# Performance work log

Hardware: AMD Instinct MI355X
Metric: run time of the kernel (lower is better)

Reference implementation:

```python
import jax, jax.numpy as jnp
import numpy as np

B, S, D_IN, D_OUT = 4, 2048, 4096, 16384


def setup_inputs() -> dict:
    key = jax.random.key(0)
    k1, k2, k3, k4 = jax.random.split(key, 4)
    x = jax.random.normal(k1, (B, S, D_IN), dtype=jnp.float32)
    # per-channel symmetric int8 weights, [out_features, in_features]
    weight_int8 = jax.random.randint(k2, (D_OUT, D_IN), -128, 128, dtype=jnp.int32).astype(jnp.int8)
    # per-channel weight scales (positive, realistic magnitude)
    weight_scale = jax.random.uniform(k3, (D_OUT,), dtype=jnp.float32) * 0.01 + 1e-4
    # static per-tensor activation scale (calibrated constant)
    act_scale = jnp.float32(0.02)
    bias = jax.random.normal(k4, (D_OUT,), dtype=jnp.float32) * 0.1
    return {"x": x, "weight_int8": weight_int8, "weight_scale": weight_scale,
            "act_scale": act_scale, "bias": bias}


def reference(x, weight_int8, weight_scale, act_scale, bias):
    orig_shape = x.shape
    orig_dtype = x.dtype
    x2d = x.reshape(-1, orig_shape[-1])  # [M, D_in]
    # static per-tensor symmetric activation quantization
    x_int8 = jnp.clip(jnp.round(x2d.astype(jnp.float32) / act_scale), -128, 127).astype(jnp.int8)
    y_int32 = jnp.matmul(x_int8, weight_int8.T, preferred_element_type=jnp.int32)  # [M, D_out]
    output_scale = (act_scale * weight_scale).astype(jnp.float32)  # [D_out]
    y = y_int32.astype(jnp.float32) * output_scale[None, :] + bias.astype(jnp.float32)[None, :]
    return y.reshape(*orig_shape[:-1], y.shape[-1]).astype(orig_dtype)
```

## Files before the change

### kernel.cpp

```cpp
#include <hip/hip_runtime.h>
#include <stdint.h>

#define GAS __attribute__((address_space(1)))
#define LAS __attribute__((address_space(3)))

typedef int v4i  __attribute__((ext_vector_type(4)));
typedef int v16i __attribute__((ext_vector_type(16)));

constexpr int Mdim = 8192;
constexpr int Ndim = 16384;
constexpr int Kdim = 4096;

__device__ __forceinline__ int pack4i8(int a, int b, int c, int d) {
    return (a & 255) | ((b & 255) << 8) | ((c & 255) << 16) | ((d & 255) << 24);
}

__device__ __forceinline__ int qz(float v, float inv) {
    return (int)fminf(fmaxf(rintf(v * inv), -128.0f), 127.0f);
}

__global__ void k_quant_x(const float* __restrict__ x, const float* __restrict__ asc,
                          int8_t* __restrict__ xq) {
    const int i = blockIdx.x * blockDim.x + threadIdx.x;
    const float inv = 1.0f / *asc;
    const float4* xv = (const float4*)x + (size_t)i * 4;
    float4 f0 = xv[0], f1 = xv[1], f2 = xv[2], f3 = xv[3];
    int4 o;
    o.x = pack4i8(qz(f0.x, inv), qz(f0.y, inv), qz(f0.z, inv), qz(f0.w, inv));
    o.y = pack4i8(qz(f1.x, inv), qz(f1.y, inv), qz(f1.z, inv), qz(f1.w, inv));
    o.z = pack4i8(qz(f2.x, inv), qz(f2.y, inv), qz(f2.z, inv), qz(f2.w, inv));
    o.w = pack4i8(qz(f3.x, inv), qz(f3.y, inv), qz(f3.z, inv), qz(f3.w, inv));
    ((int4*)xq)[i] = o;
}

__global__ void k_conv_w(const int* __restrict__ w, int8_t* __restrict__ wq) {
    const int i = blockIdx.x * blockDim.x + threadIdx.x;
    const int4* wv = (const int4*)w + (size_t)i * 4;
    int4 a = wv[0], b = wv[1], c = wv[2], d = wv[3];
    int4 o;
    o.x = pack4i8(a.x, a.y, a.z, a.w);
    o.y = pack4i8(b.x, b.y, b.z, b.w);
    o.z = pack4i8(c.x, c.y, c.z, c.w);
    o.w = pack4i8(d.x, d.y, d.z, d.w);
    ((int4*)wq)[i] = o;
}


#define VM0 asm volatile("s_waitcnt vmcnt(0)" ::: "memory")

#define RD(BUF, KS, AA, BB)                                                    \
  {                                                                            \
    _Pragma("unroll") for (int i_ = 0; i_ < 4; ++i_)                           \
      AA[i_] = *(const v4i*)(lds + (BUF) + arow + i_ * 4096 + kso[KS]);        \
    _Pragma("unroll") for (int i_ = 0; i_ < 4; ++i_)                           \
      BB[i_] = *(const v4i*)(lds + 65536 + (BUF) + brow + i_ * 4096 + kso[KS]);\
  }

#define MM(AA, BB)                                                             \
  {                                                                            \
    __builtin_amdgcn_s_setprio(1);                                             \
    _Pragma("unroll") for (int mi_ = 0; mi_ < 4; ++mi_)                        \
      _Pragma("unroll") for (int ni_ = 0; ni_ < 4; ++ni_)                      \
        acc[mi_][ni_] = __builtin_amdgcn_mfma_i32_32x32x32_i8(                 \
            AA[mi_], BB[ni_], acc[mi_][ni_], 0, 0, 0);                         \
    __builtin_amdgcn_s_setprio(0);                                             \
  }

#define TILE(T, B0, DOSTG, DORD)                                               \
  {                                                                            \
    __builtin_amdgcn_s_barrier();                                              \
    __builtin_amdgcn_sched_barrier(0);                                         \
    if (DOSTG) stage((T) + 1);                                                 \
    RD(B0, 1, aQ, bQ)                                                          \
    MM(aP, bP)                                                                 \
    RD(B0, 2, aP, bP)                                                          \
    MM(aQ, bQ)                                                                 \
    RD(B0, 3, aQ, bQ)                                                          \
    MM(aP, bP)                                                                 \
    if (DORD) {                                                                \
      VM0;                                                                     \
      __builtin_amdgcn_s_barrier();                                            \
      __builtin_amdgcn_sched_barrier(0);                                       \
      RD((B0) ^ 32768, 0, aP, bP)                                              \
    }                                                                          \
    MM(aQ, bQ)                                                                 \
  }

__global__ __launch_bounds__(256, 1)
void k_gemm32(const int8_t* __restrict__ Aq, const int8_t* __restrict__ Bq,
              const float* __restrict__ wscale, const float* __restrict__ asc,
              const float* __restrict__ bias, float* __restrict__ out) {
    __shared__ __align__(16) int8_t lds[131072];
    const int tid = threadIdx.x, lane = tid & 63, w = tid >> 6;
    const int wm = w >> 1, wn = w & 1;
    const int l5 = lane & 31, lhi = lane >> 5, llo = lane & 7;

    const int bid = blockIdx.x;
    const int swz = ((bid & 7) << 8) | (bid >> 3);
    const int mt = swz & 31, nt = swz >> 5;
    const int m0 = mt << 8, n0 = nt << 8;

    const int srow = tid >> 3;
    const int scol = (((tid & 7) ^ (srow & 7)) << 4);
    const int8_t* gA = Aq + (size_t)(m0 + srow) * Kdim + scol;
    const int8_t* gB = Bq + (size_t)(n0 + srow) * Kdim + scol;
    const size_t ustep = (size_t)32 * Kdim;
    const int dst0 = w << 10;

    auto stage = [&](int t) {
        const int buf = (t & 1) << 15;
        const int kb = t << 7;
#pragma unroll
        for (int u = 0; u < 8; ++u)
            __builtin_amdgcn_global_load_lds((const GAS void*)(gA + u * ustep + kb),
                                             (LAS void*)(lds + buf + u * 4096 + dst0), 16, 0, 0);
#pragma unroll
        for (int u = 0; u < 8; ++u)
            __builtin_amdgcn_global_load_lds((const GAS void*)(gB + u * ustep + kb),
                                             (LAS void*)(lds + 65536 + buf + u * 4096 + dst0), 16, 0, 0);
    };

    const int arow = (wm * 128 + l5) * 128;
    const int brow = (wn * 128 + l5) * 128;
    int kso[4];
#pragma unroll
    for (int ks = 0; ks < 4; ++ks) kso[ks] = (((ks * 2 + lhi) ^ llo) << 4);

    v16i acc[4][4];
#pragma unroll
    for (int i = 0; i < 4; ++i)
#pragma unroll
        for (int j = 0; j < 4; ++j)
#pragma unroll
            for (int r = 0; r < 16; ++r) acc[i][j][r] = 0;

    v4i aP[4], bP[4], aQ[4], bQ[4];

    stage(0);
    VM0;
    __builtin_amdgcn_s_barrier();
    __builtin_amdgcn_sched_barrier(0);
    RD(0, 0, aP, bP)

    for (int tt = 0; tt < 15; ++tt) {
        const int t2 = tt * 2;
        TILE(t2,     0,     1, 1)
        TILE(t2 + 1, 32768, 1, 1)
    }
    TILE(30, 0,     1, 1)
    TILE(31, 32768, 0, 0)

    const float ascale = *asc;
#pragma unroll
    for (int ni = 0; ni < 4; ++ni) {
        const int col = n0 + wn * 128 + ni * 32 + l5;
        const float sc = ascale * wscale[col];
        const float bb = bias[col];
#pragma unroll
        for (int mi = 0; mi < 4; ++mi) {
            const int rbase = m0 + wm * 128 + mi * 32 + 4 * lhi;
#pragma unroll
            for (int r = 0; r < 16; ++r) {
                const int row = rbase + (r & 3) + 8 * (r >> 2);
                out[(size_t)row * Ndim + col] = (float)acc[mi][ni][r] * sc + bb;
            }
        }
    }
}

template <bool AQ>
__global__ __launch_bounds__(256)
void k_gemm(const int8_t* __restrict__ Aq, const float* __restrict__ Xf,
            const int* __restrict__ W32,
            const float* __restrict__ wscale, const float* __restrict__ asc,
            const float* __restrict__ bias, float* __restrict__ out) {
    constexpr int BM = 128, BN = 128, BK = 64;
    constexpr int KT = Kdim / BK;
    __shared__ __align__(16) int8_t As[2][BM * BK];
    __shared__ __align__(16) int8_t Bs[2][BN * BK];

    const int tid  = threadIdx.x;
    const int lane = tid & 63;
    const int wid  = tid >> 6;
    const int wm = wid >> 1, wn = wid & 1;
    const int lrow = lane & 15, kgrp = lane >> 4;

    const int cpx = gridDim.x >> 3;
    const int swz = ((int)blockIdx.x & 7) * cpx + ((int)blockIdx.x >> 3);
    const int mt = swz & (Mdim / BM - 1);
    const int nt = swz / (Mdim / BM);
    const int m0 = mt * BM, n0 = nt * BN;

    const float ascale = *asc;
    const float inv = 1.0f / ascale;

    v4i acc[4][4];
#pragma unroll
    for (int i = 0; i < 4; ++i)
#pragma unroll
        for (int j = 0; j < 4; ++j) acc[i][j] = (v4i){0, 0, 0, 0};

    auto stg = [&](int buf, int kt) {
        const int k0 = kt * BK;
        if constexpr (AQ) {
            int8_t* ldsp = &As[buf][wid << 10];
            const int8_t* g = Aq + (size_t)(m0 + (tid >> 2)) * Kdim + k0 + ((tid & 3) << 4);
            __builtin_amdgcn_global_load_lds((const GAS void*)g, (LAS void*)ldsp, 16, 0, 0);
            __builtin_amdgcn_global_load_lds((const GAS void*)(g + (size_t)64 * Kdim),
                                             (LAS void*)(ldsp + 4096), 16, 0, 0);
        } else {
            const int row = tid >> 1, cb = (tid & 1) << 5;
            const float4* src = (const float4*)(Xf + (size_t)(m0 + row) * Kdim + k0 + cb);
            int t[8];
#pragma unroll
            for (int j = 0; j < 8; ++j) {
                float4 f = src[j];
                t[j] = pack4i8(qz(f.x, inv), qz(f.y, inv), qz(f.z, inv), qz(f.w, inv));
            }
            int4* dst = (int4*)&As[buf][row * BK + cb];
            dst[0] = make_int4(t[0], t[1], t[2], t[3]);
            dst[1] = make_int4(t[4], t[5], t[6], t[7]);
        }
        {
            const int row = tid >> 1, cb = (tid & 1) << 5;
            const int4* src = (const int4*)(W32 + (size_t)(n0 + row) * Kdim + k0 + cb);
            int t[8];
#pragma unroll
            for (int j = 0; j < 8; ++j) {
                int4 vv = src[j];
                t[j] = pack4i8(vv.x, vv.y, vv.z, vv.w);
            }
            int4* dst = (int4*)&Bs[buf][row * BK + cb];
            dst[0] = make_int4(t[0], t[1], t[2], t[3]);
            dst[1] = make_int4(t[4], t[5], t[6], t[7]);
        }
    };

    stg(0, 0);
    for (int kt = 0; kt < KT; ++kt) {
        const int cur = kt & 1;
        __syncthreads();
        if (kt + 1 < KT) stg(cur ^ 1, kt + 1);

        v4i a[4], b[4];
        const int koff = kgrp << 4;
#pragma unroll
        for (int i = 0; i < 4; ++i) {
            a[i] = *(const v4i*)&As[cur][(wm * 64 + i * 16 + lrow) * BK + koff];
            b[i] = *(const v4i*)&Bs[cur][(wn * 64 + i * 16 + lrow) * BK + koff];
        }
#pragma unroll
        for (int i = 0; i < 4; ++i)
#pragma unroll
            for (int j = 0; j < 4; ++j)
                acc[i][j] = __builtin_amdgcn_mfma_i32_16x16x64_i8(a[i], b[j], acc[i][j], 0, 0, 0);
    }

#pragma unroll
    for (int j = 0; j < 4; ++j) {
        const int col = n0 + wn * 64 + j * 16 + lrow;
        const float sc = ascale * wscale[col];
        const float bb = bias[col];
#pragma unroll
        for (int i = 0; i < 4; ++i) {
            const int r0 = m0 + wm * 64 + i * 16 + (kgrp << 2);
            float* o = out + (size_t)r0 * Ndim + col;
#pragma unroll
            for (int r = 0; r < 4; ++r)
                o[(size_t)r * Ndim] = (float)acc[i][j][r] * sc + bb;
        }
    }
}

extern "C" void kernel_launch(void* const* d_in, const int* in_sizes, int n_in,
                              void* d_out, int out_size, void* d_ws, size_t ws_size,
                              hipStream_t stream) {
    const float* x      = (const float*)d_in[0];
    const int*   w32    = (const int*)d_in[1];
    const float* wscale = (const float*)d_in[2];
    const float* asc    = (const float*)d_in[3];
    const float* bias   = (const float*)d_in[4];
    float* out = (float*)d_out;

    const size_t nx = (size_t)Mdim * Kdim;
    const size_t nw = (size_t)Ndim * Kdim;
    int8_t* xq = (int8_t*)d_ws;
    int8_t* wq = xq + nx;

    const bool haveX = ws_size >= nx;
    const bool haveW = ws_size >= nx + nw;

    if (haveX) k_quant_x<<<(int)(nx / 16 / 256), 256, 0, stream>>>(x, asc, xq);
    if (haveW) k_conv_w<<<(int)(nw / 16 / 256), 256, 0, stream>>>(w32, wq);

    if (haveW) {
        dim3 grid((Mdim / 256) * (Ndim / 256));
        k_gemm32<<<grid, 256, 0, stream>>>(xq, wq, wscale, asc, bias, out);
    } else if (haveX) {
        dim3 grid((Mdim / 128) * (Ndim / 128));
        k_gemm<true><<<grid, 256, 0, stream>>>(xq, x, w32, wscale, asc, bias, out);
    } else {
        dim3 grid((Mdim / 128) * (Ndim / 128));
        k_gemm<false><<<grid, 256, 0, stream>>>(xq, x, w32, wscale, asc, bias, out);
    }
}
```

Before: 770.6 us.

## Pre-pack operands into MFMA fragment order and stream from global to registers

The quantize and weight-convert kernels now write int8 data already laid out as per-lane MFMA fragments, in 1 KB chunks per 32-row, 32-k group. The GEMM drops its LDS staging, barriers and swizzled LDS reads. Each wave instead loads its fragments straight from global memory into registers, using a 4-deep software-pipelined register ring. This removes LDS traffic and synchronisation, but each wave loads its own copy of A and B, so operands are no longer shared between waves through LDS and global/L2 traffic rises. Latency hiding now relies only on the register prefetch distance.

```diff
diff --git a/kernel.cpp b/kernel.cpp
--- a/kernel.cpp
+++ b/kernel.cpp
@@ -10,6 +10,7 @@
 constexpr int Mdim = 8192;
 constexpr int Ndim = 16384;
 constexpr int Kdim = 4096;
+constexpr int KS   = Kdim / 32;
 
 __device__ __forceinline__ int pack4i8(int a, int b, int c, int d) {
     return (a & 255) | ((b & 255) << 8) | ((c & 255) << 16) | ((d & 255) << 24);
@@ -17,6 +18,40 @@
 
 __device__ __forceinline__ int qz(float v, float inv) {
     return (int)fminf(fmaxf(rintf(v * inv), -128.0f), 127.0f);
+}
+
+__global__ void k_quant_xf(const float* __restrict__ x, const float* __restrict__ asc,
+                           int8_t* __restrict__ xq) {
+    const int e = blockIdx.x * blockDim.x + threadIdx.x;
+    const float inv = 1.0f / *asc;
+    const int lane = e & 63, cidx = e >> 6;
+    const int ks = cidx & (KS - 1), mt32 = cidx >> 7;
+    const int row = (mt32 << 5) + (lane & 31);
+    const int k   = (ks << 5) + ((lane >> 5) << 4);
+    const float4* src = (const float4*)(x + (size_t)row * Kdim + k);
+    float4 f0 = src[0], f1 = src[1], f2 = src[2], f3 = src[3];
+    int4 o;
+    o.x = pack4i8(qz(f0.x, inv), qz(f0.y, inv), qz(f0.z, inv), qz(f0.w, inv));
+    o.y = pack4i8(qz(f1.x, inv), qz(f1.y, inv), qz(f1.z, inv), qz(f1.w, inv));
+    o.z = pack4i8(qz(f2.x, inv), qz(f2.y, inv), qz(f2.z, inv), qz(f2.w, inv));
+    o.w = pack4i8(qz(f3.x, inv), qz(f3.y, inv), qz(f3.z, inv), qz(f3.w, inv));
+    ((int4*)xq)[e] = o;
+}
+
+__global__ void k_pack_wf(const int* __restrict__ w, int8_t* __restrict__ wp) {
+    const int e = blockIdx.x * blockDim.x + threadIdx.x;
+    const int lane = e & 63, cidx = e >> 6;
+    const int ks = cidx & (KS - 1), nt32 = cidx >> 7;
+    const int n = (nt32 << 5) + (lane & 31);
+    const int k = (ks << 5) + ((lane >> 5) << 4);
+    const int4* src = (const int4*)(w + (size_t)n * Kdim + k);
+    int4 a = src[0], b = src[1], c = src[2], d = src[3];
+    int4 o;
+    o.x = pack4i8(a.x, a.y, a.z, a.w);
+    o.y = pack4i8(b.x, b.y, b.z, b.w);
+    o.z = pack4i8(c.x, c.y, c.z, c.w);
+    o.w = pack4i8(d.x, d.y, d.z, d.w);
+    ((int4*)wp)[e] = o;
 }
 
 __global__ void k_quant_x(const float* __restrict__ x, const float* __restrict__ asc,
@@ -33,98 +68,40 @@
     ((int4*)xq)[i] = o;
 }
 
-__global__ void k_conv_w(const int* __restrict__ w, int8_t* __restrict__ wq) {
-    const int i = blockIdx.x * blockDim.x + threadIdx.x;
-    const int4* wv = (const int4*)w + (size_t)i * 4;
-    int4 a = wv[0], b = wv[1], c = wv[2], d = wv[3];
-    int4 o;
-    o.x = pack4i8(a.x, a.y, a.z, a.w);
-    o.y = pack4i8(b.x, b.y, b.z, b.w);
-    o.z = pack4i8(c.x, c.y, c.z, c.w);
-    o.w = pack4i8(d.x, d.y, d.z, d.w);
-    ((int4*)wq)[i] = o;
-}
-
-
-#define VM0 asm volatile("s_waitcnt vmcnt(0)" ::: "memory")
-
-#define RD(BUF, KS, AA, BB)                                                    \
+
+#define LOADP(SET, G)                                                          \
   {                                                                            \
-    _Pragma("unroll") for (int i_ = 0; i_ < 4; ++i_)                           \
-      AA[i_] = *(const v4i*)(lds + (BUF) + arow + i_ * 4096 + kso[KS]);        \
-    _Pragma("unroll") for (int i_ = 0; i_ < 4; ++i_)                           \
-      BB[i_] = *(const v4i*)(lds + 65536 + (BUF) + brow + i_ * 4096 + kso[KS]);\
+    _Pragma("unroll") for (int q_ = 0; q_ < 4; ++q_)                           \
+      SET##a[q_] = *(const v4i*)(Apk + (((size_t)(arow32 + q_ * KS8) + (G)) << 10) + lob); \
+    _Pragma("unroll") for (int q_ = 0; q_ < 4; ++q_)                           \
+      SET##b[q_] = *(const v4i*)(Bpk + (((size_t)(brow32 + q_ * KS8) + (G)) << 10) + lob); \
   }
 
-#define MM(AA, BB)                                                             \
+#define MMP(SET)                                                               \
   {                                                                            \
-    __builtin_amdgcn_s_setprio(1);                                             \
     _Pragma("unroll") for (int mi_ = 0; mi_ < 4; ++mi_)                        \
       _Pragma("unroll") for (int ni_ = 0; ni_ < 4; ++ni_)                      \
         acc[mi_][ni_] = __builtin_amdgcn_mfma_i32_32x32x32_i8(                 \
-            AA[mi_], BB[ni_], acc[mi_][ni_], 0, 0, 0);                         \
-    __builtin_amdgcn_s_setprio(0);                                             \
+            SET##a[mi_], SET##b[ni_], acc[mi_][ni_], 0, 0, 0);                 \
   }
 
-#define TILE(T, B0, DOSTG, DORD)                                               \
-  {                                                                            \
-    __builtin_amdgcn_s_barrier();                                              \
-    __builtin_amdgcn_sched_barrier(0);                                         \
-    if (DOSTG) stage((T) + 1);                                                 \
-    RD(B0, 1, aQ, bQ)                                                          \
-    MM(aP, bP)                                                                 \
-    RD(B0, 2, aP, bP)                                                          \
-    MM(aQ, bQ)                                                                 \
-    RD(B0, 3, aQ, bQ)                                                          \
-    MM(aP, bP)                                                                 \
-    if (DORD) {                                                                \
-      VM0;                                                                     \
-      __builtin_amdgcn_s_barrier();                                            \
-      __builtin_amdgcn_sched_barrier(0);                                       \
-      RD((B0) ^ 32768, 0, aP, bP)                                              \
-    }                                                                          \
-    MM(aQ, bQ)                                                                 \
-  }
-
 __global__ __launch_bounds__(256, 1)
-void k_gemm32(const int8_t* __restrict__ Aq, const int8_t* __restrict__ Bq,
-              const float* __restrict__ wscale, const float* __restrict__ asc,
-              const float* __restrict__ bias, float* __restrict__ out) {
-    __shared__ __align__(16) int8_t lds[131072];
+void k_gemm_reg(const int8_t* __restrict__ Apk, const int8_t* __restrict__ Bpk,
+                const float* __restrict__ wscale, const float* __restrict__ asc,
+                const float* __restrict__ bias, float* __restrict__ out) {
     const int tid = threadIdx.x, lane = tid & 63, w = tid >> 6;
     const int wm = w >> 1, wn = w & 1;
-    const int l5 = lane & 31, lhi = lane >> 5, llo = lane & 7;
+    const int l5 = lane & 31, lhi = lane >> 5;
+    const int lob = lane << 4;
 
     const int bid = blockIdx.x;
     const int swz = ((bid & 7) << 8) | (bid >> 3);
     const int mt = swz & 31, nt = swz >> 5;
     const int m0 = mt << 8, n0 = nt << 8;
 
-    const int srow = tid >> 3;
-    const int scol = (((tid & 7) ^ (srow & 7)) << 4);
-    const int8_t* gA = Aq + (size_t)(m0 + srow) * Kdim + scol;
-    const int8_t* gB = Bq + (size_t)(n0 + srow) * Kdim + scol;
-    const size_t ustep = (size_t)32 * Kdim;
-    const int dst0 = w << 10;
-
-    auto stage = [&](int t) {
-        const int buf = (t & 1) << 15;
-        const int kb = t << 7;
-#pragma unroll
-        for (int u = 0; u < 8; ++u)
-            __builtin_amdgcn_global_load_lds((const GAS void*)(gA + u * ustep + kb),
-                                             (LAS void*)(lds + buf + u * 4096 + dst0), 16, 0, 0);
-#pragma unroll
-        for (int u = 0; u < 8; ++u)
-            __builtin_amdgcn_global_load_lds((const GAS void*)(gB + u * ustep + kb),
-                                             (LAS void*)(lds + 65536 + buf + u * 4096 + dst0), 16, 0, 0);
-    };
-
-    const int arow = (wm * 128 + l5) * 128;
-    const int brow = (wn * 128 + l5) * 128;
-    int kso[4];
-#pragma unroll
-    for (int ks = 0; ks < 4; ++ks) kso[ks] = (((ks * 2 + lhi) ^ llo) << 4);
+    constexpr int KS8 = KS;
+    const int arow32 = ((m0 >> 5) + (wm << 2)) * KS;
+    const int brow32 = ((n0 >> 5) + (wn << 2)) * KS;
 
     v16i acc[4][4];
 #pragma unroll
@@ -134,21 +111,21 @@
 #pragma unroll
             for (int r = 0; r < 16; ++r) acc[i][j][r] = 0;
 
-    v4i aP[4], bP[4], aQ[4], bQ[4];
-
-    stage(0);
-    VM0;
-    __builtin_amdgcn_s_barrier();
-    __builtin_amdgcn_sched_barrier(0);
-    RD(0, 0, aP, bP)
-
-    for (int tt = 0; tt < 15; ++tt) {
-        const int t2 = tt * 2;
-        TILE(t2,     0,     1, 1)
-        TILE(t2 + 1, 32768, 1, 1)
-    }
-    TILE(30, 0,     1, 1)
-    TILE(31, 32768, 0, 0)
+    v4i S0a[4], S0b[4], S1a[4], S1b[4], S2a[4], S2b[4], S3a[4], S3b[4];
+
+    LOADP(S0, 0)
+    LOADP(S1, 1)
+
+    for (int g = 0; g < 124; g += 4) {
+        LOADP(S2, g + 2)  MMP(S0)
+        LOADP(S3, g + 3)  MMP(S1)
+        LOADP(S0, g + 4)  MMP(S2)
+        LOADP(S1, g + 5)  MMP(S3)
+    }
+    LOADP(S2, 126)  MMP(S0)
+    LOADP(S3, 127)  MMP(S1)
+    MMP(S2)
+    MMP(S3)
 
     const float ascale = *asc;
 #pragma unroll
@@ -285,18 +262,18 @@
     const size_t nx = (size_t)Mdim * Kdim;
     const size_t nw = (size_t)Ndim * Kdim;
     int8_t* xq = (int8_t*)d_ws;
-    int8_t* wq = xq + nx;
+    int8_t* wp = xq + nx;
 
     const bool haveX = ws_size >= nx;
     const bool haveW = ws_size >= nx + nw;
 
-    if (haveX) k_quant_x<<<(int)(nx / 16 / 256), 256, 0, stream>>>(x, asc, xq);
-    if (haveW) k_conv_w<<<(int)(nw / 16 / 256), 256, 0, stream>>>(w32, wq);
-
     if (haveW) {
+        k_quant_xf<<<(int)(nx / 16 / 256), 256, 0, stream>>>(x, asc, xq);
+        k_pack_wf<<<(int)(nw / 16 / 256), 256, 0, stream>>>(w32, wp);
         dim3 grid((Mdim / 256) * (Ndim / 256));
-        k_gemm32<<<grid, 256, 0, stream>>>(xq, wq, wscale, asc, bias, out);
+        k_gemm_reg<<<grid, 256, 0, stream>>>(xq, wp, wscale, asc, bias, out);
     } else if (haveX) {
+        k_quant_x<<<(int)(nx / 16 / 256), 256, 0, stream>>>(x, asc, xq);
         dim3 grid((Mdim / 128) * (Ndim / 128));
         k_gemm<true><<<grid, 256, 0, stream>>>(xq, x, w32, wscale, asc, bias, out);
     } else {
```

After: 1.041 ms. +35.1%, slower.
